# Kernel optimization log

Measured on AMD Instinct MI355X. Metric: run time of the kernel, lower is better.

Reference implementation:

```python
import jax, jax.numpy as jnp
import numpy as np

N_NODES = 100000
N_EDGES = 1600000
N_GRAPHS = 2048
F_IN = 33
D = 256


def _graph_conv(x, edge_index, w_rel, b_rel, w_root):
    # PyG GraphConv (aggr='add'): out = lin_rel(sum_j x_j) + lin_root(x)
    src, dst = edge_index[0], edge_index[1]
    agg = jax.ops.segment_sum(x[src], dst, num_segments=x.shape[0])  # [N, F]
    return agg @ w_rel + b_rel + x @ w_root


def setup_inputs() -> dict:
    key = jax.random.key(0)
    ks = jax.random.split(key, 16)
    scale_in = 1.0 / np.sqrt(F_IN)
    scale_d = 1.0 / np.sqrt(D)
    inp = {
        "x": jax.random.normal(ks[0], (N_NODES, F_IN), dtype=jnp.float32),
        "edge_index": jax.random.randint(ks[1], (2, N_EDGES), 0, N_NODES),
        "batch_index": jnp.sort(jax.random.randint(ks[2], (N_NODES,), 0, N_GRAPHS)),
        # initial_conv: GraphConv(F_IN -> D)
        "w_rel0": jax.random.normal(ks[3], (F_IN, D), dtype=jnp.float32) * scale_in,
        "b_rel0": jnp.zeros((D,), dtype=jnp.float32),
        "w_root0": jax.random.normal(ks[4], (F_IN, D), dtype=jnp.float32) * scale_in,
        # conv1..conv3: GraphConv(D -> D)
        "w_rel1": jax.random.normal(ks[5], (D, D), dtype=jnp.float32) * scale_d,
        "b_rel1": jnp.zeros((D,), dtype=jnp.float32),
        "w_root1": jax.random.normal(ks[6], (D, D), dtype=jnp.float32) * scale_d,
        "w_rel2": jax.random.normal(ks[7], (D, D), dtype=jnp.float32) * scale_d,
        "b_rel2": jnp.zeros((D,), dtype=jnp.float32),
        "w_root2": jax.random.normal(ks[8], (D, D), dtype=jnp.float32) * scale_d,
        "w_rel3": jax.random.normal(ks[9], (D, D), dtype=jnp.float32) * scale_d,
        "b_rel3": jnp.zeros((D,), dtype=jnp.float32),
        "w_root3": jax.random.normal(ks[10], (D, D), dtype=jnp.float32) * scale_d,
        # output head Linear(D -> 1)
        "w_out": jax.random.normal(ks[11], (D, 1), dtype=jnp.float32) * scale_d,
        "b_out": jnp.zeros((1,), dtype=jnp.float32),
    }
    return inp


def reference(x, edge_index, batch_index,
              w_rel0, b_rel0, w_root0,
              w_rel1, b_rel1, w_root1,
              w_rel2, b_rel2, w_root2,
              w_rel3, b_rel3, w_root3,
              w_out, b_out):
    # dropout omitted (eval mode)
    h = jax.nn.gelu(_graph_conv(x, edge_index, w_rel0, b_rel0, w_root0))
    h = jax.nn.gelu(_graph_conv(h, edge_index, w_rel1, b_rel1, w_root1))
    h = jax.nn.gelu(_graph_conv(h, edge_index, w_rel2, b_rel2, w_root2))
    h = jax.nn.gelu(_graph_conv(h, edge_index, w_rel3, b_rel3, w_root3))
    # global mean pool over graphs
    sums = jax.ops.segment_sum(h, batch_index, num_segments=N_GRAPHS)          # [G, D]
    counts = jax.ops.segment_sum(jnp.ones((h.shape[0],), h.dtype), batch_index,
                                 num_segments=N_GRAPHS)                         # [G]
    pooled = sums / jnp.maximum(counts, 1.0)[:, None]
    return pooled @ w_out + b_out                                               # [G, 1]
```

## Files before the change

kernel.cpp:

```cpp
#include <hip/hip_runtime.h>
#include <math.h>

#define NN 100000
#define NE 1600000
#define NG 2048
#define FIN 33
#define DD 256

#define SH 8
#define NB ((NN + 255) >> 8)
#define CH 4096
#define PCAP 4608
#define ESCAP 6144

#define RBLKS ((NN + 255) / 256)

typedef __attribute__((ext_vector_type(8))) short bf16x8;
typedef __attribute__((ext_vector_type(4))) float f32x4;

__device__ __forceinline__ float b2f(unsigned short u){
    union { unsigned int i; float f; } c; c.i = ((unsigned int)u) << 16; return c.f;
}
__device__ __forceinline__ unsigned short f2b(float f){
    union { float f; unsigned int u; } c; c.f = f;
    unsigned int r = c.u + 0x7fffu + ((c.u >> 16) & 1u);
    return (unsigned short)(r >> 16);
}

__device__ __forceinline__ float gelu_tanh(float x){
    float z = 0.7978845608028654f * (x + 0.044715f * x * x * x);
    return x / (1.0f + __expf(-2.0f * z));
}

__global__ __launch_bounds__(256) void k_bin(const int* __restrict__ src,
                                             const int* __restrict__ dst,
                                             int* __restrict__ gcur,
                                             int* __restrict__ pairs){
    __shared__ int cnt[NB];
    __shared__ int lb[NB];
    __shared__ int gbase[NB];
    __shared__ int sc[512];
    __shared__ int2 stage[CH];

    int t = threadIdx.x;
    for(int i = t; i < NB; i += 256) cnt[i] = 0;
    __syncthreads();

    int e0 = blockIdx.x * CH;
    int n = NE - e0; if(n > CH) n = CH;

    int  myb[16];
    int  myr[16];
    int2 myp[16];
    #pragma unroll
    for(int k = 0; k < 16; k++){
        int e = e0 + t + k * 256;
        if(e < NE){
            int s = src[e], d = dst[e];
            int b = d >> SH;
            myr[k] = atomicAdd(&cnt[b], 1);
            myb[k] = b;
            myp[k] = make_int2(s, d);
        } else myb[k] = -1;
    }
    __syncthreads();

    sc[t]       = (t       < NB) ? cnt[t]       : 0;
    sc[t + 256] = (t + 256 < NB) ? cnt[t + 256] : 0;
    __syncthreads();
    for(int off = 1; off < 512; off <<= 1){
        int a  = (t >= off)       ? sc[t - off]       : 0;
        int b2 = (t + 256 >= off) ? sc[t + 256 - off] : 0;
        __syncthreads();
        sc[t] += a; sc[t + 256] += b2;
        __syncthreads();
    }
    for(int i = t; i < NB; i += 256){
        lb[i] = sc[i] - cnt[i];
        int c = cnt[i];
        gbase[i] = (c > 0) ? atomicAdd(&gcur[i], c) : 0;
    }
    __syncthreads();

    #pragma unroll
    for(int k = 0; k < 16; k++){
        if(myb[k] >= 0) stage[lb[myb[k]] + myr[k]] = myp[k];
    }
    __syncthreads();

    for(int i = t; i < n; i += 256){
        int2 p = stage[i];
        int b = p.y >> SH;
        int tgt = gbase[b] + (i - lb[b]);
        if(tgt < PCAP) pairs[(size_t)b * PCAP + tgt] = p.x | ((p.y & 255) << 17);
    }
}

__global__ void k_sscan(const int* __restrict__ gcur, int* __restrict__ boff){
    __shared__ int s[512];
    int t = threadIdx.x;
    int v = 0;
    if(t < NB){ v = gcur[t]; if(v > PCAP) v = PCAP; }
    s[t] = v; __syncthreads();
    for(int off = 1; off < 512; off <<= 1){
        int u = (t >= off) ? s[t - off] : 0;
        __syncthreads();
        s[t] += u;
        __syncthreads();
    }
    if(t < NB) boff[t] = s[t] - v;
}

__global__ __launch_bounds__(256) void k_bcsr(const int* __restrict__ pairs,
                                              const int* __restrict__ gcur,
                                              const int* __restrict__ boff,
                                              int* __restrict__ deg,
                                              int* __restrict__ rs,
                                              int* __restrict__ esrc){
    __shared__ int hist[256];
    __shared__ int sc[256];
    __shared__ int cur2[256];
    __shared__ int est[ESCAP];

    int b = blockIdx.x;
    int t = threadIdx.x;
    int m = gcur[b]; if(m > PCAP) m = PCAP;
    int pstart = boff[b];
    const int* bp = pairs + (size_t)b * PCAP;

    hist[t] = 0;
    __syncthreads();
    for(int i = t; i < m; i += 256) atomicAdd(&hist[(bp[i] >> 17) & 255], 1);
    __syncthreads();

    sc[t] = hist[t]; __syncthreads();
    for(int off = 1; off < 256; off <<= 1){
        int u = (t >= off) ? sc[t - off] : 0;
        __syncthreads();
        sc[t] += u;
        __syncthreads();
    }
    int excl = sc[t] - hist[t];
    cur2[t] = excl;
    int node = (b << 8) + t;
    if(node < NN){
        deg[node] = hist[t];
        rs[node]  = pstart + excl;
    }
    __syncthreads();

    for(int i = t; i < m; i += 256){
        int p = bp[i];
        int pos = atomicAdd(&cur2[(p >> 17) & 255], 1);
        int s = p & 0x1FFFF;
        if(pos < ESCAP) est[pos] = s;
        else esrc[pstart + pos] = s;
    }
    __syncthreads();
    int lim = (m < ESCAP) ? m : ESCAP;
    for(int i = t; i < lim; i += 256) esrc[pstart + i] = est[i];
}

__global__ void k_xpad(const float* __restrict__ x, unsigned short* __restrict__ xb){
    int idx = blockIdx.x * 256 + threadIdx.x;
    if(idx >= NN * 64) return;
    int n = idx >> 6, c = idx & 63;
    xb[idx] = (c < FIN) ? f2b(x[(size_t)n * FIN + c]) : 0;
}

__global__ void k_aggx(const unsigned short* __restrict__ xb, const int* __restrict__ rs,
                       const int* __restrict__ deg, const int* __restrict__ esrc,
                       unsigned short* __restrict__ axb){
    int wv = (blockIdx.x * blockDim.x + threadIdx.x) >> 6;
    int lane = threadIdx.x & 63;
    int node = wv * 4 + (lane >> 4);
    int l16 = lane & 15;
    if(node >= NN) return;
    int start = rs[node], cnt = deg[node];
    float a0 = 0.f, a1 = 0.f, a2 = 0.f, a3 = 0.f;
    const unsigned short* xp = xb + l16 * 4;
    int j = 0;
    for(; j + 4 <= cnt; j += 4){
        int e0 = esrc[start+j], e1 = esrc[start+j+1], e2 = esrc[start+j+2], e3 = esrc[start+j+3];
        ushort4 v0 = *(const ushort4*)(xp + (size_t)e0 * 64);
        ushort4 v1 = *(const ushort4*)(xp + (size_t)e1 * 64);
        ushort4 v2 = *(const ushort4*)(xp + (size_t)e2 * 64);
        ushort4 v3 = *(const ushort4*)(xp + (size_t)e3 * 64);
        a0 += (b2f(v0.x) + b2f(v1.x)) + (b2f(v2.x) + b2f(v3.x));
        a1 += (b2f(v0.y) + b2f(v1.y)) + (b2f(v2.y) + b2f(v3.y));
        a2 += (b2f(v0.z) + b2f(v1.z)) + (b2f(v2.z) + b2f(v3.z));
        a3 += (b2f(v0.w) + b2f(v1.w)) + (b2f(v2.w) + b2f(v3.w));
    }
    for(; j < cnt; j++){
        int e = esrc[start + j];
        ushort4 v = *(const ushort4*)(xp + (size_t)e * 64);
        a0 += b2f(v.x); a1 += b2f(v.y); a2 += b2f(v.z); a3 += b2f(v.w);
    }
    ushort4 o; o.x = f2b(a0); o.y = f2b(a1); o.z = f2b(a2); o.w = f2b(a3);
    *(ushort4*)(axb + (size_t)node * 64 + l16 * 4) = o;
}

__global__ void k_agg256(const unsigned short* __restrict__ h, const int* __restrict__ rs,
                         const int* __restrict__ deg, const int* __restrict__ esrc,
                         unsigned short* __restrict__ agg){
    int wv = (blockIdx.x * blockDim.x + threadIdx.x) >> 6;
    int lane = threadIdx.x & 63;
    int node = wv * 2 + (lane >> 5);
    int l32 = lane & 31;
    if(node >= NN) return;
    int start = rs[node], cnt = deg[node];
    float a[8] = {0.f,0.f,0.f,0.f,0.f,0.f,0.f,0.f};
    const unsigned short* hp = h + l32 * 8;
    int j = 0;
    for(; j + 8 <= cnt; j += 8){
        bf16x8 v[8];
        #pragma unroll
        for(int q = 0; q < 8; q++){
            int e = esrc[start + j + q];
            v[q] = *(const bf16x8*)(hp + (size_t)e * DD);
        }
        #pragma unroll
        for(int q = 0; q < 8; q++)
            #pragma unroll
            for(int d = 0; d < 8; d++)
                a[d] += b2f((unsigned short)v[q][d]);
    }
    for(; j < cnt; j++){
        int e = esrc[start + j];
        bf16x8 v = *(const bf16x8*)(hp + (size_t)e * DD);
        #pragma unroll
        for(int d = 0; d < 8; d++) a[d] += b2f((unsigned short)v[d]);
    }
    bf16x8 o;
    #pragma unroll
    for(int d = 0; d < 8; d++) o[d] = (short)f2b(a[d]);
    *(bf16x8*)(agg + (size_t)node * DD + l32 * 8) = o;
}

struct WPtrs { const float* w[6]; };

__global__ void k_wt6(WPtrs wp, unsigned short* __restrict__ btAll){
    __shared__ float s[16][17];
    const float* W = wp.w[blockIdx.z];
    unsigned short* Bt = btAll + (size_t)blockIdx.z * DD * DD;
    int tx = threadIdx.x, ty = threadIdx.y;
    int k = blockIdx.y * 16 + ty;
    int j = blockIdx.x * 16 + tx;
    s[ty][tx] = W[k * DD + j];
    __syncthreads();
    Bt[(size_t)(blockIdx.x * 16 + ty) * DD + blockIdx.y * 16 + tx] = f2b(s[tx][ty]);
}

struct W2Ptrs { const float* w[2]; };

__global__ void k_wt0(W2Ptrs wp, unsigned short* __restrict__ btAll){
    int idx = blockIdx.x * 256 + threadIdx.x;
    if(idx >= DD * 64) return;
    const float* W = wp.w[blockIdx.z];
    unsigned short* Bt = btAll + (size_t)blockIdx.z * DD * 64;
    int j = idx >> 6, k = idx & 63;
    Bt[idx] = (k < FIN) ? f2b(W[(size_t)k * DD + j]) : 0;
}

__global__ void k_cnt(const int* __restrict__ batch, int* __restrict__ gcnt){
    int i = blockIdx.x * 256 + threadIdx.x;
    if(i < NN) atomicAdd(&gcnt[batch[i]], 1);
}

template<int KS, int AST, bool POOL>
__global__ __launch_bounds__(512, 4) void k_mfma_gemm(
    const unsigned short* __restrict__ A0, const unsigned short* __restrict__ A1,
    const unsigned short* __restrict__ Bt0, const unsigned short* __restrict__ Bt1,
    const float* __restrict__ bias, unsigned short* __restrict__ out,
    const int* __restrict__ batch, const float* __restrict__ wout,
    float* __restrict__ gsum)
{
    constexpr int CK  = KS * 32;
    constexpr int BST = CK + 8;
    constexpr int SEG = CK / 8;
    __shared__ unsigned short Bs[128 * BST];

    int t = threadIdx.x;
    int lane = t & 63;
    int w = t >> 6;
    int r16 = lane & 15;
    int kg  = lane >> 4;

    int bid = blockIdx.x;
    int rblk = (bid >> 4) * 8 + (bid & 7);
    int chalf = (bid >> 3) & 1;
    if(rblk >= RBLKS) return;
    int i0 = rblk * 256;
    int jbase = chalf * 128;
    int baseRow = i0 + w * 32;

    f32x4 acc[2][8];
    #pragma unroll
    for(int m = 0; m < 2; m++)
        #pragma unroll
        for(int n = 0; n < 8; n++)
            acc[m][n] = (f32x4){0.f, 0.f, 0.f, 0.f};

    auto loadA = [&](int gks, bf16x8* af){
        const unsigned short* Ap = (gks < KS) ? A0 : A1;
        int kk = ((gks < KS) ? gks : gks - KS) * 32 + kg * 8;
        #pragma unroll
        for(int m = 0; m < 2; m++){
            int gi = baseRow + m * 16 + r16;
            if(gi > NN - 1) gi = NN - 1;
            af[m] = *(const bf16x8*)(Ap + (size_t)gi * AST + kk);
        }
    };

    bf16x8 afb[4][2];
    loadA(0, afb[0]);
    loadA(1, afb[1]);
    if(2 < 2 * KS) loadA(2, afb[2]);
    if(3 < 2 * KS) loadA(3, afb[3]);

    #pragma unroll
    for(int c = 0; c < 2; c++){
        const unsigned short* Bp = c ? Bt1 : Bt0;
        if(c) __syncthreads();
        #pragma unroll
        for(int p = 0; p < (128 * SEG) / 512; p++){
            int idx = p * 512 + t;
            int row = idx / SEG;
            int k8 = (idx % SEG) * 8;
            *(bf16x8*)(&Bs[row * BST + k8]) =
                *(const bf16x8*)(Bp + (size_t)(jbase + row) * AST + k8);
        }
        __syncthreads();
        #pragma unroll
        for(int ksl = 0; ksl < KS; ksl++){
            int gks = c * KS + ksl;
            #pragma unroll
            for(int n = 0; n < 8; n++){
                bf16x8 bfr = *(const bf16x8*)(&Bs[(n * 16 + r16) * BST + ksl * 32 + kg * 8]);
                acc[0][n] = __builtin_amdgcn_mfma_f32_16x16x32_bf16(afb[gks & 3][0], bfr, acc[0][n], 0, 0, 0);
                acc[1][n] = __builtin_amdgcn_mfma_f32_16x16x32_bf16(afb[gks & 3][1], bfr, acc[1][n], 0, 0, 0);
            }
            if(gks + 4 < 2 * KS) loadA(gks + 4, afb[gks & 3]);
        }
    }

    int rg = kg * 4;
    if constexpr (!POOL){
        #pragma unroll
        for(int n = 0; n < 8; n++){
            int gj = jbase + n * 16 + r16;
            float bb = bias[gj];
            #pragma unroll
            for(int m = 0; m < 2; m++){
                #pragma unroll
                for(int r = 0; r < 4; r++){
                    int gi = baseRow + m * 16 + rg + r;
                    if(gi < NN)
                        out[(size_t)gi * DD + gj] = f2b(gelu_tanh(acc[m][n][r] + bb));
                }
            }
        }
    } else {
        #pragma unroll
        for(int m = 0; m < 2; m++){
            #pragma unroll
            for(int r = 0; r < 4; r++){
                float s = 0.f;
                #pragma unroll
                for(int n = 0; n < 8; n++){
                    int gj = jbase + n * 16 + r16;
                    s += gelu_tanh(acc[m][n][r] + bias[gj]) * wout[gj];
                }
                s += __shfl_xor(s, 1);
                s += __shfl_xor(s, 2);
                s += __shfl_xor(s, 4);
                s += __shfl_xor(s, 8);
                int gi = baseRow + m * 16 + rg + r;
                if(r16 == 0 && gi < NN)
                    atomicAdd(&gsum[batch[gi]], s);
            }
        }
    }
}

__global__ void k_final(const float* __restrict__ gsum, const int* __restrict__ gcnt,
                        const float* __restrict__ bout, float* __restrict__ out){
    int g = blockIdx.x * 256 + threadIdx.x;
    if(g < NG) out[g] = gsum[g] / fmaxf((float)gcnt[g], 1.f) + bout[0];
}

extern "C" void kernel_launch(void* const* d_in, const int* in_sizes, int n_in,
                              void* d_out, int out_size, void* d_ws, size_t ws_size,
                              hipStream_t stream){
    const float* x       = (const float*)d_in[0];
    const int*   ei      = (const int*)d_in[1];
    const int*   src     = ei;
    const int*   dst     = ei + NE;
    const int*   batch   = (const int*)d_in[2];
    const float* w_rel0  = (const float*)d_in[3];
    const float* b_rel0  = (const float*)d_in[4];
    const float* w_root0 = (const float*)d_in[5];
    const float* w_rel1  = (const float*)d_in[6];
    const float* b_rel1  = (const float*)d_in[7];
    const float* w_root1 = (const float*)d_in[8];
    const float* w_rel2  = (const float*)d_in[9];
    const float* b_rel2  = (const float*)d_in[10];
    const float* w_root2 = (const float*)d_in[11];
    const float* w_rel3  = (const float*)d_in[12];
    const float* b_rel3  = (const float*)d_in[13];
    const float* w_root3 = (const float*)d_in[14];
    const float* w_out   = (const float*)d_in[15];
    const float* b_out   = (const float*)d_in[16];
    float* out = (float*)d_out;

    char* ws = (char*)d_ws;
    size_t off = 0;
    auto alloc = [&](size_t bytes) -> void* {
        void* p = ws + off;
        off = (off + bytes + 255) & ~(size_t)255;
        return p;
    };
    unsigned short* hA  = (unsigned short*)alloc((size_t)NN * DD * 2);
    unsigned short* hB  = (unsigned short*)alloc((size_t)NN * DD * 2);
    unsigned short* agg = (unsigned short*)alloc((size_t)NN * DD * 2);
    int*   deg  = (int*)alloc((size_t)NN * 4);
    int*   rs   = (int*)alloc((size_t)NN * 4);
    int*   esrc = (int*)alloc((size_t)NE * 4);
    int*   gcur = (int*)alloc(512 * 4);
    int*   boff = (int*)alloc(512 * 4);
    float* gsum = (float*)alloc((size_t)NG * 4);
    int*   gcnt = (int*)alloc((size_t)NG * 4);
    unsigned short* btAll = (unsigned short*)alloc((size_t)6 * DD * DD * 2);
    unsigned short* bt0All = (unsigned short*)alloc((size_t)2 * DD * 64 * 2);
    (void)ws_size; (void)in_sizes; (void)n_in; (void)out_size;

    int* pairs = (int*)hB;
    unsigned short* xb  = agg;
    unsigned short* axb = agg + (size_t)NN * 64 + 128;

    hipMemsetAsync(gcur, 0, 512 * 4, stream);
    k_bin<<<(NE + CH - 1) / CH, 256, 0, stream>>>(src, dst, gcur, pairs);
    k_sscan<<<1, 512, 0, stream>>>(gcur, boff);
    k_bcsr<<<NB, 256, 0, stream>>>(pairs, gcur, boff, deg, rs, esrc);

    size_t poolBytes = (size_t)((char*)(gcnt + NG) - (char*)gsum);
    hipMemsetAsync(gsum, 0, poolBytes, stream);
    k_cnt<<<(NN + 255) / 256, 256, 0, stream>>>(batch, gcnt);

    WPtrs wp; wp.w[0] = w_rel1; wp.w[1] = w_root1; wp.w[2] = w_rel2;
    wp.w[3] = w_root2; wp.w[4] = w_rel3; wp.w[5] = w_root3;
    k_wt6<<<dim3(16, 16, 6), dim3(16, 16), 0, stream>>>(wp, btAll);
    W2Ptrs w2; w2.w[0] = w_rel0; w2.w[1] = w_root0;
    k_wt0<<<dim3((DD * 64 + 255) / 256, 1, 2), 256, 0, stream>>>(w2, bt0All);
    k_xpad<<<(NN * 64 + 255) / 256, 256, 0, stream>>>(x, xb);

    unsigned short* bt[6];
    for(int i = 0; i < 6; i++) bt[i] = btAll + (size_t)i * DD * DD;
    unsigned short* bt0r = bt0All;
    unsigned short* bt0o = bt0All + (size_t)DD * 64;

    int agg2Grid = (NN * 32 + 255) / 256;
    int gemmGrid = ((RBLKS + 7) / 8) * 16;

    k_aggx<<<(NN + 15) / 16, 256, 0, stream>>>(xb, rs, deg, esrc, axb);
    k_mfma_gemm<2, 64, false><<<gemmGrid, 512, 0, stream>>>(axb, xb, bt0r, bt0o, b_rel0, hA,
                                                            batch, w_out, gsum);
    k_agg256<<<agg2Grid, 256, 0, stream>>>(hA, rs, deg, esrc, agg);
    k_mfma_gemm<8, 256, false><<<gemmGrid, 512, 0, stream>>>(agg, hA, bt[0], bt[1], b_rel1, hB,
                                                             batch, w_out, gsum);
    k_agg256<<<agg2Grid, 256, 0, stream>>>(hB, rs, deg, esrc, agg);
    k_mfma_gemm<8, 256, false><<<gemmGrid, 512, 0, stream>>>(agg, hB, bt[2], bt[3], b_rel2, hA,
                                                             batch, w_out, gsum);
    k_agg256<<<agg2Grid, 256, 0, stream>>>(hA, rs, deg, esrc, agg);
    k_mfma_gemm<8, 256, true><<<gemmGrid, 512, 0, stream>>>(agg, hA, bt[4], bt[5], b_rel3, hB,
                                                            batch, w_out, gsum);

    k_final<<<(NG + 255) / 256, 256, 0, stream>>>(gsum, gcnt, b_out, out);
}
```

Before: 749.6 us.

## Restructure GEMM to 128x128 tiles with direct global-to-LDS loads for A and B

Rewrites the fused GraphConv GEMM kernel. Tiles shrink from 256x128 to 128x128 per block with 4 waves, each owning a 64x64 sub-tile. Both A and B are now staged in LDS one 32-wide K slice at a time using global_load_lds, replacing direct register loads of A and a whole-K B panel. The aim is better operand reuse per wave and smaller LDS so more blocks fit per CU. The cost is a barrier per K slice with no double buffering, so load latency is no longer overlapped with MFMA work.

```diff
diff --git a/kernel.cpp b/kernel.cpp
--- a/kernel.cpp
+++ b/kernel.cpp
@@ -13,7 +13,7 @@
 #define PCAP 4608
 #define ESCAP 6144
 
-#define RBLKS ((NN + 255) / 256)
+#define FB2 ((NN + 127) / 128)
 
 typedef __attribute__((ext_vector_type(8))) short bf16x8;
 typedef __attribute__((ext_vector_type(4))) float f32x4;
@@ -30,6 +30,12 @@
 __device__ __forceinline__ float gelu_tanh(float x){
     float z = 0.7978845608028654f * (x + 0.044715f * x * x * x);
     return x / (1.0f + __expf(-2.0f * z));
+}
+
+__device__ __forceinline__ void gload_lds16(const unsigned short* g, unsigned short* l){
+    __builtin_amdgcn_global_load_lds(
+        (const __attribute__((address_space(1))) void*)g,
+        (__attribute__((address_space(3))) void*)l, 16, 0, 0);
 }
 
 __global__ __launch_bounds__(256) void k_bin(const int* __restrict__ src,
@@ -268,17 +274,15 @@
 }
 
 template<int KS, int AST, bool POOL>
-__global__ __launch_bounds__(512, 4) void k_mfma_gemm(
+__global__ __launch_bounds__(256, 3) void k_mfma_gemm(
     const unsigned short* __restrict__ A0, const unsigned short* __restrict__ A1,
     const unsigned short* __restrict__ Bt0, const unsigned short* __restrict__ Bt1,
     const float* __restrict__ bias, unsigned short* __restrict__ out,
     const int* __restrict__ batch, const float* __restrict__ wout,
     float* __restrict__ gsum)
 {
-    constexpr int CK  = KS * 32;
-    constexpr int BST = CK + 8;
-    constexpr int SEG = CK / 8;
-    __shared__ unsigned short Bs[128 * BST];
+    __shared__ unsigned short As[128 * 32];
+    __shared__ unsigned short Bs[128 * 32];
 
     int t = threadIdx.x;
     int lane = t & 63;
@@ -289,72 +293,65 @@
     int bid = blockIdx.x;
     int rblk = (bid >> 4) * 8 + (bid & 7);
     int chalf = (bid >> 3) & 1;
-    if(rblk >= RBLKS) return;
-    int i0 = rblk * 256;
+    if(rblk >= FB2) return;
+    int i0 = rblk * 128;
     int jbase = chalf * 128;
-    int baseRow = i0 + w * 32;
-
-    f32x4 acc[2][8];
+
+    int wm = (w >> 1) * 64;
+    int wn = (w & 1) * 64;
+
+    f32x4 acc[4][4];
     #pragma unroll
-    for(int m = 0; m < 2; m++)
-        #pragma unroll
-        for(int n = 0; n < 8; n++)
+    for(int m = 0; m < 4; m++)
+        #pragma unroll
+        for(int n = 0; n < 4; n++)
             acc[m][n] = (f32x4){0.f, 0.f, 0.f, 0.f};
 
-    auto loadA = [&](int gks, bf16x8* af){
+    int srow = lane >> 2;
+    int skc  = (lane & 3) * 8;
+
+    for(int gks = 0; gks < 2 * KS; gks++){
         const unsigned short* Ap = (gks < KS) ? A0 : A1;
-        int kk = ((gks < KS) ? gks : gks - KS) * 32 + kg * 8;
-        #pragma unroll
-        for(int m = 0; m < 2; m++){
-            int gi = baseRow + m * 16 + r16;
-            if(gi > NN - 1) gi = NN - 1;
-            af[m] = *(const bf16x8*)(Ap + (size_t)gi * AST + kk);
+        const unsigned short* Bp = (gks < KS) ? Bt0 : Bt1;
+        int kk = ((gks < KS) ? gks : gks - KS) * 32;
+
+        if(gks) __syncthreads();
+        #pragma unroll
+        for(int q = 0; q < 2; q++){
+            int row = w * 32 + q * 16 + srow;
+            int gia = i0 + row; if(gia > NN - 1) gia = NN - 1;
+            gload_lds16(Ap + (size_t)gia * AST + kk + skc,
+                        As + (w * 32 + q * 16) * 32);
+            gload_lds16(Bp + (size_t)(jbase + row) * AST + kk + skc,
+                        Bs + (w * 32 + q * 16) * 32);
         }
-    };
-
-    bf16x8 afb[4][2];
-    loadA(0, afb[0]);
-    loadA(1, afb[1]);
-    if(2 < 2 * KS) loadA(2, afb[2]);
-    if(3 < 2 * KS) loadA(3, afb[3]);
-
-    #pragma unroll
-    for(int c = 0; c < 2; c++){
-        const unsigned short* Bp = c ? Bt1 : Bt0;
-        if(c) __syncthreads();
-        #pragma unroll
-        for(int p = 0; p < (128 * SEG) / 512; p++){
-            int idx = p * 512 + t;
-            int row = idx / SEG;
-            int k8 = (idx % SEG) * 8;
-            *(bf16x8*)(&Bs[row * BST + k8]) =
-                *(const bf16x8*)(Bp + (size_t)(jbase + row) * AST + k8);
-        }
-        __syncthreads();
-        #pragma unroll
-        for(int ksl = 0; ksl < KS; ksl++){
-            int gks = c * KS + ksl;
+        __syncthreads();
+
+        bf16x8 af[4], bfr[4];
+        #pragma unroll
+        for(int m = 0; m < 4; m++)
+            af[m] = *(const bf16x8*)(As + (wm + m * 16 + r16) * 32 + kg * 8);
+        #pragma unroll
+        for(int n = 0; n < 4; n++)
+            bfr[n] = *(const bf16x8*)(Bs + (wn + n * 16 + r16) * 32 + kg * 8);
+        #pragma unroll
+        for(int m = 0; m < 4; m++)
             #pragma unroll
-            for(int n = 0; n < 8; n++){
-                bf16x8 bfr = *(const bf16x8*)(&Bs[(n * 16 + r16) * BST + ksl * 32 + kg * 8]);
-                acc[0][n] = __builtin_amdgcn_mfma_f32_16x16x32_bf16(afb[gks & 3][0], bfr, acc[0][n], 0, 0, 0);
-                acc[1][n] = __builtin_amdgcn_mfma_f32_16x16x32_bf16(afb[gks & 3][1], bfr, acc[1][n], 0, 0, 0);
-            }
-            if(gks + 4 < 2 * KS) loadA(gks + 4, afb[gks & 3]);
-        }
+            for(int n = 0; n < 4; n++)
+                acc[m][n] = __builtin_amdgcn_mfma_f32_16x16x32_bf16(af[m], bfr[n], acc[m][n], 0, 0, 0);
     }
 
     int rg = kg * 4;
     if constexpr (!POOL){
         #pragma unroll
-        for(int n = 0; n < 8; n++){
-            int gj = jbase + n * 16 + r16;
+        for(int n = 0; n < 4; n++){
+            int gj = jbase + wn + n * 16 + r16;
             float bb = bias[gj];
             #pragma unroll
-            for(int m = 0; m < 2; m++){
+            for(int m = 0; m < 4; m++){
                 #pragma unroll
                 for(int r = 0; r < 4; r++){
-                    int gi = baseRow + m * 16 + rg + r;
+                    int gi = i0 + wm + m * 16 + rg + r;
                     if(gi < NN)
                         out[(size_t)gi * DD + gj] = f2b(gelu_tanh(acc[m][n][r] + bb));
                 }
@@ -362,20 +359,20 @@
         }
     } else {
         #pragma unroll
-        for(int m = 0; m < 2; m++){
+        for(int m = 0; m < 4; m++){
             #pragma unroll
             for(int r = 0; r < 4; r++){
                 float s = 0.f;
                 #pragma unroll
-                for(int n = 0; n < 8; n++){
-                    int gj = jbase + n * 16 + r16;
+                for(int n = 0; n < 4; n++){
+                    int gj = jbase + wn + n * 16 + r16;
                     s += gelu_tanh(acc[m][n][r] + bias[gj]) * wout[gj];
                 }
                 s += __shfl_xor(s, 1);
                 s += __shfl_xor(s, 2);
                 s += __shfl_xor(s, 4);
                 s += __shfl_xor(s, 8);
-                int gi = baseRow + m * 16 + rg + r;
+                int gi = i0 + wm + m * 16 + rg + r;
                 if(r16 == 0 && gi < NN)
                     atomicAdd(&gsum[batch[gi]], s);
             }
@@ -460,19 +457,19 @@
     unsigned short* bt0o = bt0All + (size_t)DD * 64;
 
     int agg2Grid = (NN * 32 + 255) / 256;
-    int gemmGrid = ((RBLKS + 7) / 8) * 16;
+    int gemmGrid = ((FB2 + 7) / 8) * 16;
 
     k_aggx<<<(NN + 15) / 16, 256, 0, stream>>>(xb, rs, deg, esrc, axb);
-    k_mfma_gemm<2, 64, false><<<gemmGrid, 512, 0, stream>>>(axb, xb, bt0r, bt0o, b_rel0, hA,
+    k_mfma_gemm<2, 64, false><<<gemmGrid, 256, 0, stream>>>(axb, xb, bt0r, bt0o, b_rel0, hA,
                                                             batch, w_out, gsum);
     k_agg256<<<agg2Grid, 256, 0, stream>>>(hA, rs, deg, esrc, agg);
-    k_mfma_gemm<8, 256, false><<<gemmGrid, 512, 0, stream>>>(agg, hA, bt[0], bt[1], b_rel1, hB,
+    k_mfma_gemm<8, 256, false><<<gemmGrid, 256, 0, stream>>>(agg, hA, bt[0], bt[1], b_rel1, hB,
                                                              batch, w_out, gsum);
     k_agg256<<<agg2Grid, 256, 0, stream>>>(hB, rs, deg, esrc, agg);
-    k_mfma_gemm<8, 256, false><<<gemmGrid, 512, 0, stream>>>(agg, hB, bt[2], bt[3], b_rel2, hA,
+    k_mfma_gemm<8, 256, false><<<gemmGrid, 256, 0, stream>>>(agg, hB, bt[2], bt[3], b_rel2, hA,
                                                              batch, w_out, gsum);
     k_agg256<<<agg2Grid, 256, 0, stream>>>(hA, rs, deg, esrc, agg);
-    k_mfma_gemm<8, 256, true><<<gemmGrid, 512, 0, stream>>>(agg, hA, bt[4], bt[5], b_rel3, hB,
+    k_mfma_gemm<8, 256, true><<<gemmGrid, 256, 0, stream>>>(agg, hA, bt[4], bt[5], b_rel3, hB,
                                                             batch, w_out, gsum);
 
     k_final<<<(NG + 255) / 256, 256, 0, stream>>>(gsum, gcnt, b_out, out);
```

Measured after the change: 815.5 us. 8.8% more time.

## Overlap neighbor aggregation with root GEMM in a heterogeneous kernel

Applied to the files above, without the earlier changes.

Splits each 256-wide GraphConv layer into a heterogeneous kernel and a relation GEMM. The heterogeneous kernel interleaves blocks that do the memory-bound neighbor aggregation with blocks that compute the root-weight GEMM plus bias into a bf16 buffer. A second kernel then computes the aggregation GEMM, adds the stored root result, and applies GELU or pooling. The aim is to hide the compute-light gather behind MFMA work, at the cost of an extra bf16 round trip of the root partial, which adds memory traffic and a second rounding step.

```diff
diff --git a/kernel.cpp b/kernel.cpp
--- a/kernel.cpp
+++ b/kernel.cpp
@@ -14,6 +14,8 @@
 #define ESCAP 6144
 
 #define RBLKS ((NN + 255) / 256)
+#define NAGG  ((NN + 15) / 16)
+#define NGEM  (RBLKS * 2)
 
 typedef __attribute__((ext_vector_type(8))) short bf16x8;
 typedef __attribute__((ext_vector_type(4))) float f32x4;
@@ -200,43 +202,6 @@
     *(ushort4*)(axb + (size_t)node * 64 + l16 * 4) = o;
 }
 
-__global__ void k_agg256(const unsigned short* __restrict__ h, const int* __restrict__ rs,
-                         const int* __restrict__ deg, const int* __restrict__ esrc,
-                         unsigned short* __restrict__ agg){
-    int wv = (blockIdx.x * blockDim.x + threadIdx.x) >> 6;
-    int lane = threadIdx.x & 63;
-    int node = wv * 2 + (lane >> 5);
-    int l32 = lane & 31;
-    if(node >= NN) return;
-    int start = rs[node], cnt = deg[node];
-    float a[8] = {0.f,0.f,0.f,0.f,0.f,0.f,0.f,0.f};
-    const unsigned short* hp = h + l32 * 8;
-    int j = 0;
-    for(; j + 8 <= cnt; j += 8){
-        bf16x8 v[8];
-        #pragma unroll
-        for(int q = 0; q < 8; q++){
-            int e = esrc[start + j + q];
-            v[q] = *(const bf16x8*)(hp + (size_t)e * DD);
-        }
-        #pragma unroll
-        for(int q = 0; q < 8; q++)
-            #pragma unroll
-            for(int d = 0; d < 8; d++)
-                a[d] += b2f((unsigned short)v[q][d]);
-    }
-    for(; j < cnt; j++){
-        int e = esrc[start + j];
-        bf16x8 v = *(const bf16x8*)(hp + (size_t)e * DD);
-        #pragma unroll
-        for(int d = 0; d < 8; d++) a[d] += b2f((unsigned short)v[d]);
-    }
-    bf16x8 o;
-    #pragma unroll
-    for(int d = 0; d < 8; d++) o[d] = (short)f2b(a[d]);
-    *(bf16x8*)(agg + (size_t)node * DD + l32 * 8) = o;
-}
-
 struct WPtrs { const float* w[6]; };
 
 __global__ void k_wt6(WPtrs wp, unsigned short* __restrict__ btAll){
@@ -267,13 +232,11 @@
     if(i < NN) atomicAdd(&gcnt[batch[i]], 1);
 }
 
-template<int KS, int AST, bool POOL>
-__global__ __launch_bounds__(512, 4) void k_mfma_gemm(
+template<int KS, int AST>
+__global__ __launch_bounds__(512, 4) void k_gemm0(
     const unsigned short* __restrict__ A0, const unsigned short* __restrict__ A1,
     const unsigned short* __restrict__ Bt0, const unsigned short* __restrict__ Bt1,
-    const float* __restrict__ bias, unsigned short* __restrict__ out,
-    const int* __restrict__ batch, const float* __restrict__ wout,
-    float* __restrict__ gsum)
+    const float* __restrict__ bias, unsigned short* __restrict__ out)
 {
     constexpr int CK  = KS * 32;
     constexpr int BST = CK + 8;
@@ -345,7 +308,118 @@
     }
 
     int rg = kg * 4;
-    if constexpr (!POOL){
+    #pragma unroll
+    for(int n = 0; n < 8; n++){
+        int gj = jbase + n * 16 + r16;
+        float bb = bias[gj];
+        #pragma unroll
+        for(int m = 0; m < 2; m++){
+            #pragma unroll
+            for(int r = 0; r < 4; r++){
+                int gi = baseRow + m * 16 + rg + r;
+                if(gi < NN)
+                    out[(size_t)gi * DD + gj] = f2b(gelu_tanh(acc[m][n][r] + bb));
+            }
+        }
+    }
+}
+
+__global__ __launch_bounds__(512, 2) void k_het(
+    const unsigned short* __restrict__ h,
+    const int* __restrict__ rs, const int* __restrict__ deg, const int* __restrict__ esrc,
+    unsigned short* __restrict__ aggout,
+    const unsigned short* __restrict__ BtRoot,
+    const float* __restrict__ bias,
+    unsigned short* __restrict__ R)
+{
+    __shared__ unsigned short Bs[128 * 264];
+
+    int bid = blockIdx.x;
+    int q = bid / 9, rr = bid % 9;
+    int t = threadIdx.x;
+    int lane = t & 63;
+    int w = t >> 6;
+
+    if(rr < 8){
+        int aggIdx = q * 8 + rr;
+        int node = aggIdx * 16 + w * 2 + (lane >> 5);
+        int l32 = lane & 31;
+        if(node >= NN) return;
+        int start = rs[node], cnt = deg[node];
+        float a[8] = {0.f,0.f,0.f,0.f,0.f,0.f,0.f,0.f};
+        const unsigned short* hp = h + l32 * 8;
+        int j = 0;
+        for(; j + 8 <= cnt; j += 8){
+            bf16x8 v[8];
+            #pragma unroll
+            for(int qq = 0; qq < 8; qq++){
+                int e = esrc[start + j + qq];
+                v[qq] = *(const bf16x8*)(hp + (size_t)e * DD);
+            }
+            #pragma unroll
+            for(int qq = 0; qq < 8; qq++)
+                #pragma unroll
+                for(int d = 0; d < 8; d++)
+                    a[d] += b2f((unsigned short)v[qq][d]);
+        }
+        for(; j < cnt; j++){
+            int e = esrc[start + j];
+            bf16x8 v = *(const bf16x8*)(hp + (size_t)e * DD);
+            #pragma unroll
+            for(int d = 0; d < 8; d++) a[d] += b2f((unsigned short)v[d]);
+        }
+        bf16x8 o;
+        #pragma unroll
+        for(int d = 0; d < 8; d++) o[d] = (short)f2b(a[d]);
+        *(bf16x8*)(aggout + (size_t)node * DD + l32 * 8) = o;
+    } else {
+        int gemmIdx = q;
+        int rblk = gemmIdx >> 1, chalf = gemmIdx & 1;
+        int i0 = rblk * 256, jbase = chalf * 128;
+        int r16 = lane & 15, kg = lane >> 4;
+        int baseRow = i0 + w * 32;
+
+        f32x4 acc[2][8];
+        #pragma unroll
+        for(int m = 0; m < 2; m++)
+            #pragma unroll
+            for(int n = 0; n < 8; n++)
+                acc[m][n] = (f32x4){0.f, 0.f, 0.f, 0.f};
+
+        auto loadA = [&](int ks, bf16x8* af){
+            int kk = ks * 32 + kg * 8;
+            #pragma unroll
+            for(int m = 0; m < 2; m++){
+                int gi = baseRow + m * 16 + r16;
+                if(gi > NN - 1) gi = NN - 1;
+                af[m] = *(const bf16x8*)(h + (size_t)gi * DD + kk);
+            }
+        };
+        bf16x8 afb[4][2];
+        loadA(0, afb[0]); loadA(1, afb[1]); loadA(2, afb[2]); loadA(3, afb[3]);
+
+        #pragma unroll
+        for(int p = 0; p < 8; p++){
+            int idx = p * 512 + t;
+            int row = idx >> 5;
+            int k8 = (idx & 31) * 8;
+            *(bf16x8*)(&Bs[row * 264 + k8]) =
+                *(const bf16x8*)(BtRoot + (size_t)(jbase + row) * DD + k8);
+        }
+        __syncthreads();
+
+        #pragma unroll
+        for(int ks = 0; ks < 8; ks++){
+            #pragma unroll
+            for(int n = 0; n < 8; n++){
+                bf16x8 bfr = *(const bf16x8*)(&Bs[(n * 16 + r16) * 264 + ks * 32 + kg * 8]);
+                acc[0][n] = __builtin_amdgcn_mfma_f32_16x16x32_bf16(afb[ks & 3][0], bfr, acc[0][n], 0, 0, 0);
+                acc[1][n] = __builtin_amdgcn_mfma_f32_16x16x32_bf16(afb[ks & 3][1], bfr, acc[1][n], 0, 0, 0);
+            }
+            if(ks + 4 < 8) loadA(ks + 4, afb[ks & 3]);
+        }
+
+        int rg = kg * 4;
         #pragma unroll
         for(int n = 0; n < 8; n++){
             int gj = jbase + n * 16 + r16;
@@ -356,26 +430,107 @@
                 for(int r = 0; r < 4; r++){
                     int gi = baseRow + m * 16 + rg + r;
                     if(gi < NN)
-                        out[(size_t)gi * DD + gj] = f2b(gelu_tanh(acc[m][n][r] + bb));
+                        R[(size_t)gi * DD + gj] = f2b(acc[m][n][r] + bb);
                 }
             }
         }
+    }
+}
+
+template<bool POOL>
+__global__ __launch_bounds__(512, 2) void k_rel(
+    const unsigned short* __restrict__ aggin,
+    const unsigned short* __restrict__ BtRel,
+    unsigned short* __restrict__ R,
+    const int* __restrict__ batch, const float* __restrict__ wout,
+    float* __restrict__ gsum)
+{
+    __shared__ unsigned short Bs[128 * 264];
+
+    int t = threadIdx.x;
+    int lane = t & 63;
+    int w = t >> 6;
+    int r16 = lane & 15, kg = lane >> 4;
+
+    int gemmIdx = blockIdx.x;
+    int rblk = gemmIdx >> 1, chalf = gemmIdx & 1;
+    int i0 = rblk * 256, jbase = chalf * 128;
+    int baseRow = i0 + w * 32;
+
+    f32x4 acc[2][8];
+    #pragma unroll
+    for(int m = 0; m < 2; m++)
+        #pragma unroll
+        for(int n = 0; n < 8; n++)
+            acc[m][n] = (f32x4){0.f, 0.f, 0.f, 0.f};
+
+    auto loadA = [&](int ks, bf16x8* af){
+        int kk = ks * 32 + kg * 8;
+        #pragma unroll
+        for(int m = 0; m < 2; m++){
+            int gi = baseRow + m * 16 + r16;
+            if(gi > NN - 1) gi = NN - 1;
+            af[m] = *(const bf16x8*)(aggin + (size_t)gi * DD + kk);
+        }
+    };
+    bf16x8 afb[4][2];
+    loadA(0, afb[0]); loadA(1, afb[1]); loadA(2, afb[2]); loadA(3, afb[3]);
+
+    #pragma unroll
+    for(int p = 0; p < 8; p++){
+        int idx = p * 512 + t;
+        int row = idx >> 5;
+        int k8 = (idx & 31) * 8;
+        *(bf16x8*)(&Bs[row * 264 + k8]) =
+            *(const bf16x8*)(BtRel + (size_t)(jbase + row) * DD + k8);
+    }
+    __syncthreads();
+
+    #pragma unroll
+    for(int ks = 0; ks < 8; ks++){
+        #pragma unroll
+        for(int n = 0; n < 8; n++){
+            bf16x8 bfr = *(const bf16x8*)(&Bs[(n * 16 + r16) * 264 + ks * 32 + kg * 8]);
+            acc[0][n] = __builtin_amdgcn_mfma_f32_16x16x32_bf16(afb[ks & 3][0], bfr, acc[0][n], 0, 0, 0);
+            acc[1][n] = __builtin_amdgcn_mfma_f32_16x16x32_bf16(afb[ks & 3][1], bfr, acc[1][n], 0, 0, 0);
+        }
+        if(ks + 4 < 8) loadA(ks + 4, afb[ks & 3]);
+    }
+
+    int rg = kg * 4;
+    if constexpr (!POOL){
+        #pragma unroll
+        for(int n = 0; n < 8; n++){
+            int gj = jbase + n * 16 + r16;
+            #pragma unroll
+            for(int m = 0; m < 2; m++){
+                #pragma unroll
+                for(int r = 0; r < 4; r++){
+                    int gi = baseRow + m * 16 + rg + r;
+                    if(gi < NN){
+                        size_t adr = (size_t)gi * DD + gj;
+                        R[adr] = f2b(gelu_tanh(acc[m][n][r] + b2f(R[adr])));
+                    }
+                }
+            }
+        }
     } else {
         #pragma unroll
         for(int m = 0; m < 2; m++){
             #pragma unroll
             for(int r = 0; r < 4; r++){
+                int gi = baseRow + m * 16 + rg + r;
                 float s = 0.f;
                 #pragma unroll
                 for(int n = 0; n < 8; n++){
                     int gj = jbase + n * 16 + r16;
-                    s += gelu_tanh(acc[m][n][r] + bias[gj]) * wout[gj];
+                    float rv = (gi < NN) ? b2f(R[(size_t)gi * DD + gj]) : 0.f;
+                    s += gelu_tanh(acc[m][n][r] + rv) * wout[gj];
                 }
                 s += __shfl_xor(s, 1);
                 s += __shfl_xor(s, 2);
                 s += __shfl_xor(s, 4);
                 s += __shfl_xor(s, 8);
-                int gi = baseRow + m * 16 + rg + r;
                 if(r16 == 0 && gi < NN)
                     atomicAdd(&gsum[batch[gi]], s);
             }
@@ -459,21 +614,18 @@
     unsigned short* bt0r = bt0All;
     unsigned short* bt0o = bt0All + (size_t)DD * 64;
 
-    int agg2Grid = (NN * 32 + 255) / 256;
-    int gemmGrid = ((RBLKS + 7) / 8) * 16;
+    int gemm0Grid = ((RBLKS + 7) / 8) * 16;
+    int hetGrid = NGEM * 9;
 
     k_aggx<<<(NN + 15) / 16, 256, 0, stream>>>(xb, rs, deg, esrc, axb);
-    k_mfma_gemm<2, 64, false><<<gemmGrid, 512, 0, stream>>>(axb, xb, bt0r, bt0o, b_rel0, hA,
-                                                            batch, w_out, gsum);
-    k_agg256<<<agg2Grid, 256, 0, stream>>>(hA, rs, deg, esrc, agg);
-    k_mfma_gemm<8, 256, false><<<gemmGrid, 512, 0, stream>>>(agg, hA, bt[0], bt[1], b_rel1, hB,
-                                                             batch, w_out, gsum);
-    k_agg256<<<agg2Grid, 256, 0, stream>>>(hB, rs, deg, esrc, agg);
-    k_mfma_gemm<8, 256, false><<<gemmGrid, 512, 0, stream>>>(agg, hB, bt[2], bt[3], b_rel2, hA,
-                                                             batch, w_out, gsum);
-    k_agg256<<<agg2Grid, 256, 0, stream>>>(hA, rs, deg, esrc, agg);
-    k_mfma_gemm<8, 256, true><<<gemmGrid, 512, 0, stream>>>(agg, hA, bt[4], bt[5], b_rel3, hB,
-                                                            batch, w_out, gsum);
+    k_gemm0<2, 64><<<gemm0Grid, 512, 0, stream>>>(axb, xb, bt0r, bt0o, b_rel0, hA);
+
+    k_het<<<hetGrid, 512, 0, stream>>>(hA, rs, deg, esrc, agg, bt[1], b_rel1, hB);
+    k_rel<false><<<NGEM, 512, 0, stream>>>(agg, bt[0], hB, batch, w_out, gsum);
+    k_het<<<hetGrid, 512, 0, stream>>>(hB, rs, deg, esrc, agg, bt[3], b_rel2, hA);
+    k_rel<false><<<NGEM, 512, 0, stream>>>(agg, bt[2], hA, batch, w_out, gsum);
+    k_het<<<hetGrid, 512, 0, stream>>>(hA, rs, deg, esrc, agg, bt[5], b_rel3, hB);
+    k_rel<true><<<NGEM, 512, 0, stream>>>(agg, bt[4], hB, batch, w_out, gsum);
 
     k_final<<<(NG + 255) / 256, 256, 0, stream>>>(gsum, gcnt, b_out, out);
 }
```

Measured after the change: 883.3 us. 1.18x slower.
